# Performance work log

Measured on AMD Instinct MI355X. Metric: run time of the kernel, lower is better.

Reference implementation:

```python
import jax, jax.numpy as jnp
import numpy as np

B, S, H = 4, 2048, 1024
NH, HD = 16, 64
FF = 4096
EPS = 1e-5

def _ln(x, g, b):
    m = jnp.mean(x, axis=-1, keepdims=True)
    v = jnp.var(x, axis=-1, keepdims=True)
    return (x - m) * jax.lax.rsqrt(v + EPS) * g + b

def setup_inputs() -> dict:
    key = jax.random.key(0)
    ks = jax.random.split(key, 12)
    sc = 0.02
    return {
        "hidden_states": jax.random.normal(ks[0], (B, S, H), jnp.float32),
        "Wq": jax.random.normal(ks[1], (H, H), jnp.float32) * sc,
        "bq": jnp.zeros((H,), jnp.float32),
        "Wk": jax.random.normal(ks[2], (H, H), jnp.float32) * sc,
        "bk": jnp.zeros((H,), jnp.float32),
        "Wv": jax.random.normal(ks[3], (H, H), jnp.float32) * sc,
        "bv": jnp.zeros((H,), jnp.float32),
        "Wi": jax.random.normal(ks[4], (H, FF), jnp.float32) * sc,
        "bi": jnp.zeros((FF,), jnp.float32),
        "Wo": jax.random.normal(ks[5], (FF, H), jnp.float32) * sc,
        "bo": jnp.zeros((H,), jnp.float32),
        "g1": jnp.ones((H,), jnp.float32),
        "b1": jnp.zeros((H,), jnp.float32),
        "g2": jnp.ones((H,), jnp.float32),
        "b2": jnp.zeros((H,), jnp.float32),
    }

def reference(hidden_states, Wq, bq, Wk, bk, Wv, bv, Wi, bi, Wo, bo, g1, b1, g2, b2):
    x = hidden_states
    # projections -> [B, NH, S, HD]
    def split(t):
        return t.reshape(B, S, NH, HD).transpose(0, 2, 1, 3)
    q = split(x @ Wq + bq)
    k = split(x @ Wk + bk)
    v = split(x @ Wv + bv)
    scores = jnp.einsum('bhqd,bhkd->bhqk', q, k) / jnp.sqrt(jnp.float32(HD))
    probs = jax.nn.softmax(scores, axis=-1)
    ctx = jnp.einsum('bhqk,bhkd->bhqd', probs, v)
    attn_out = ctx.transpose(0, 2, 1, 3).reshape(B, S, H)
    h = _ln(x + attn_out, g1, b1)
    ffn = jax.nn.gelu(h @ Wi + bi, approximate=False) @ Wo + bo
    return _ln(h + ffn, g2, b2)
```

## Files before the change

kernel.cpp:

```cpp
#include <hip/hip_runtime.h>

#define B_  4
#define S_  2048
#define H_  1024
#define NH_ 16
#define HD_ 64
#define FF_ 4096
#define M_  (B_*S_)

typedef __bf16 bf16x8 __attribute__((ext_vector_type(8)));
typedef float  f32x4  __attribute__((ext_vector_type(4)));
typedef unsigned short ushort8v __attribute__((ext_vector_type(8)));
typedef unsigned short ushort4v __attribute__((ext_vector_type(4)));

typedef __attribute__((address_space(1))) void GVOID;
typedef __attribute__((address_space(3))) void LVOID;

__device__ __forceinline__ void g2l16(const void* g, void* l) {
  __builtin_amdgcn_global_load_lds((GVOID*)g, (LVOID*)l, 16, 0, 0);
}

#define MFMA16(a, b, c) __builtin_amdgcn_mfma_f32_16x16x32_bf16(a, b, c, 0, 0, 0)

#if __has_builtin(__builtin_amdgcn_exp2f)
#define EXP2(x) __builtin_amdgcn_exp2f(x)
#else
#define EXP2(x) exp2f(x)
#endif

__device__ __forceinline__ unsigned short f2bf(float f) {
  unsigned int u = __float_as_uint(f);
  u += 0x7fffu + ((u >> 16) & 1u);
  return (unsigned short)(u >> 16);
}
__device__ __forceinline__ float bf2f(unsigned short h) {
  return __uint_as_float(((unsigned int)h) << 16);
}

__device__ __forceinline__ void xcd_swz(int& bx, int& by) {
  int gx = gridDim.x;
  int flat = by * gx + bx;
  int cpx = (gx * gridDim.y) >> 3;
  int swz = (flat & 7) * cpx + (flat >> 3);
  bx = swz % gx;
  by = swz / gx;
}

__device__ __forceinline__ void xcd_swzT(int& bx, int& by) {
  int gy = gridDim.y;
  int flat = bx * gy + by;
  int cpx = (gridDim.x * gy) >> 3;
  int swz = (flat & 7) * cpx + (flat >> 3);
  by = swz % gy;
  bx = swz / gy;
}

__global__ __launch_bounds__(256) void cast_f32_bf16(const float* __restrict__ in,
                                                     unsigned short* __restrict__ out,
                                                     int n4) {
  int i = blockIdx.x * 256 + threadIdx.x;
  if (i >= n4) return;
  float4 v = reinterpret_cast<const float4*>(in)[i];
  ushort4v o;
  o[0] = f2bf(v.x); o[1] = f2bf(v.y); o[2] = f2bf(v.z); o[3] = f2bf(v.w);
  reinterpret_cast<ushort4v*>(out)[i] = o;
}

__global__ __launch_bounds__(256) void transpose_cast(const float* __restrict__ in,
                                                      unsigned short* __restrict__ out,
                                                      int R, int C) {
  __shared__ float t[32][33];
  const int bx = blockIdx.x * 32;
  const int by = blockIdx.y * 32;
  const int tx = threadIdx.x & 31, ty = threadIdx.x >> 5;
#pragma unroll
  for (int i = 0; i < 32; i += 8)
    t[ty + i][tx] = in[(size_t)(by + ty + i) * C + bx + tx];
  __syncthreads();
#pragma unroll
  for (int i = 0; i < 32; i += 8)
    out[(size_t)(bx + ty + i) * R + by + tx] = f2bf(t[tx][ty + i]);
}

__global__ __launch_bounds__(256) void transpose_cast3(const float* __restrict__ i0,
                                                       const float* __restrict__ i1,
                                                       const float* __restrict__ i2,
                                                       unsigned short* __restrict__ o0,
                                                       unsigned short* __restrict__ o1,
                                                       unsigned short* __restrict__ o2) {
  __shared__ float t[32][33];
  const float* in = (blockIdx.z == 0) ? i0 : (blockIdx.z == 1) ? i1 : i2;
  unsigned short* out = (blockIdx.z == 0) ? o0 : (blockIdx.z == 1) ? o1 : o2;
  const int bx = blockIdx.x * 32;
  const int by = blockIdx.y * 32;
  const int tx = threadIdx.x & 31, ty = threadIdx.x >> 5;
#pragma unroll
  for (int i = 0; i < 32; i += 8)
    t[ty + i][tx] = in[(size_t)(by + ty + i) * H_ + bx + tx];
  __syncthreads();
#pragma unroll
  for (int i = 0; i < 32; i += 8)
    out[(size_t)(bx + ty + i) * H_ + by + tx] = f2bf(t[tx][ty + i]);
}

#define ALOAD(bufv, mf, ks)                                                      \
  *reinterpret_cast<const bf16x8*>((char*)As + (bufv)*32768 + wm*16384 +         \
      ((mf)*16 + lr)*128 + (((((ks)*4 + kg)) ^ (lr & 7)) * 16))
#define BLOAD(bufv, nf, ks)                                                      \
  *reinterpret_cast<const bf16x8*>((char*)Bs + (bufv)*32768 + bh*16384 +         \
      (brow0 + (nf)*16 + lr)*128 + (((((ks)*4 + kg)) ^ (lr & 7)) * 16))

#define PH_MFMA(MF0)                                                             \
  __builtin_amdgcn_s_barrier();                                                  \
  asm volatile("s_waitcnt lgkmcnt(0)" ::: "memory");                             \
  __builtin_amdgcn_s_setprio(1);                                                 \
  _Pragma("unroll")                                                              \
  for (int nf = 0; nf < 4; ++nf) {                                               \
    acc[MF0][nf]     = MFMA16(a_[0][0], bfr[nf][0], acc[MF0][nf]);               \
    acc[MF0][nf]     = MFMA16(a_[0][1], bfr[nf][1], acc[MF0][nf]);               \
    acc[MF0 + 1][nf] = MFMA16(a_[1][0], bfr[nf][0], acc[MF0 + 1][nf]);           \
    acc[MF0 + 1][nf] = MFMA16(a_[1][1], bfr[nf][1], acc[MF0 + 1][nf]);           \
  }                                                                              \
  __builtin_amdgcn_s_setprio(0);

#define GEMM256_CORE(A_, Bt_, LDK_, NKT_, KOFF_)                                 \
  __shared__ unsigned short As[2][2][128 * 64];                                  \
  __shared__ unsigned short Bs[2][2][128 * 64];                                  \
  const int tid  = threadIdx.x;                                                  \
  const int wave = tid >> 6;                                                     \
  const int lane = tid & 63;                                                     \
  const int kg   = lane >> 4;                                                    \
  const int lr   = lane & 15;                                                    \
  const int wm   = wave >> 2;                                                    \
  const int wn   = wave & 3;                                                     \
  const int bh   = wn >> 1;                                                      \
  const int brow0 = (wn & 1) * 64;                                               \
  const int sr = lane >> 3;                                                      \
  const int sc = ((lane & 7) ^ sr) * 8;                                          \
  const unsigned short* sA = &A_[(size_t)(m0 + wave * 8 + sr) * LDK_ + KOFF_ + sc];  \
  const unsigned short* sB = &Bt_[(size_t)(n0 + wave * 8 + sr) * LDK_ + KOFF_ + sc]; \
  char* ldsA = (char*)&As[0][0][0] + wave * 1024;                                \
  char* ldsB = (char*)&Bs[0][0][0] + wave * 1024;                                \
  const size_t rkI = (size_t)64 * LDK_;                                          \
  const size_t rhK = (size_t)128 * LDK_;                                         \
  f32x4 acc[8][4] = {};                                                          \
  const int nkt = (NKT_);                                                        \
  g2l16(sA,             ldsA);                                                   \
  g2l16(sA + rkI,       ldsA + 8192);                                            \
  g2l16(sA + rhK,       ldsA + 16384);                                           \
  g2l16(sA + rhK + rkI, ldsA + 16384 + 8192);                                    \
  g2l16(sB,             ldsB);                                                   \
  g2l16(sB + rkI,       ldsB + 8192);                                            \
  g2l16(sB + rhK,       ldsB + 16384);                                           \
  g2l16(sB + rhK + rkI, ldsB + 16384 + 8192);                                    \
  g2l16(sB + 64,             ldsB + 32768);                                      \
  g2l16(sB + rkI + 64,       ldsB + 32768 + 8192);                               \
  g2l16(sB + rhK + 64,       ldsB + 32768 + 16384);                              \
  g2l16(sB + rhK + rkI + 64, ldsB + 32768 + 16384 + 8192);                       \
  asm volatile("s_waitcnt vmcnt(4)" ::: "memory");                               \
  __builtin_amdgcn_s_barrier();                                                  \
  for (int c = 0; c < nkt; ++c) {                                                \
    const int buf = c & 1;                                                       \
    const bool stgA = (c + 1 < nkt);                                             \
    const bool stgB = (c + 2 < nkt);                                             \
    const size_t kA = (size_t)(c + 1) * 64;                                      \
    const size_t kB = (size_t)(c + 2) * 64;                                      \
    bf16x8 bfr[4][2];                                                            \
    bf16x8 a_[2][2];                                                             \
    _Pragma("unroll")                                                            \
    for (int nf = 0; nf < 4; ++nf) {                                             \
      bfr[nf][0] = BLOAD(buf, nf, 0);                                            \
      bfr[nf][1] = BLOAD(buf, nf, 1);                                            \
    }                                                                            \
    a_[0][0] = ALOAD(buf, 0, 0); a_[0][1] = ALOAD(buf, 0, 1);                    \
    a_[1][0] = ALOAD(buf, 1, 0); a_[1][1] = ALOAD(buf, 1, 1);                    \
    if (stgA) {                                                                  \
      g2l16(sA + kA,       ldsA + (buf ^ 1) * 32768);                            \
      g2l16(sA + rkI + kA, ldsA + (buf ^ 1) * 32768 + 8192);                     \
    }                                                                            \
    PH_MFMA(0)                                                                   \
    __builtin_amdgcn_s_barrier();                                                \
    a_[0][0] = ALOAD(buf, 2, 0); a_[0][1] = ALOAD(buf, 2, 1);                    \
    a_[1][0] = ALOAD(buf, 3, 0); a_[1][1] = ALOAD(buf, 3, 1);                    \
    if (stgA) {                                                                  \
      g2l16(sA + rhK + kA,       ldsA + (buf ^ 1) * 32768 + 16384);              \
      g2l16(sA + rhK + rkI + kA, ldsA + (buf ^ 1) * 32768 + 16384 + 8192);       \
    }                                                                            \
    PH_MFMA(2)                                                                   \
    __builtin_amdgcn_s_barrier();                                                \
    a_[0][0] = ALOAD(buf, 4, 0); a_[0][1] = ALOAD(buf, 4, 1);                    \
    a_[1][0] = ALOAD(buf, 5, 0); a_[1][1] = ALOAD(buf, 5, 1);                    \
    if (stgB) {                                                                  \
      g2l16(sB + kB,       ldsB + buf * 32768);                                  \
      g2l16(sB + rkI + kB, ldsB + buf * 32768 + 8192);                           \
    }                                                                            \
    PH_MFMA(4)                                                                   \
    __builtin_amdgcn_s_barrier();                                                \
    a_[0][0] = ALOAD(buf, 6, 0); a_[0][1] = ALOAD(buf, 6, 1);                    \
    a_[1][0] = ALOAD(buf, 7, 0); a_[1][1] = ALOAD(buf, 7, 1);                    \
    if (stgB) {                                                                  \
      g2l16(sB + rhK + kB,       ldsB + buf * 32768 + 16384);                    \
      g2l16(sB + rhK + rkI + kB, ldsB + buf * 32768 + 16384 + 8192);             \
    }                                                                            \
    PH_MFMA(6)                                                                   \
    if (c < nkt - 2)       asm volatile("s_waitcnt vmcnt(4)" ::: "memory");      \
    else if (c == nkt - 2) asm volatile("s_waitcnt vmcnt(0)" ::: "memory");      \
    __builtin_amdgcn_s_barrier();                                                \
  }

template<int ACT, int OUT_F32>
__global__ __launch_bounds__(512, 1) void gemm256_tn(const unsigned short* __restrict__ A,
                                                     const unsigned short* __restrict__ Bt,
                                                     const float* __restrict__ bias,
                                                     void* __restrict__ C,
                                                     int M, int N, int K) {
  int bx = blockIdx.x, by = blockIdx.y;
  xcd_swzT(bx, by);
  const int z = blockIdx.z;
  const int Klen = K / gridDim.z;
  const int Koff = z * Klen;
  const float* biasEff = (z == 0) ? bias : nullptr;
  const int m0 = bx * 256;
  const int n0 = by * 256;
  GEMM256_CORE(A, Bt, K, Klen >> 6, Koff)

  float* Cf = (float*)C + (size_t)z * M * N;
#pragma unroll
  for (int mf = 0; mf < 8; ++mf) {
#pragma unroll
    for (int nf = 0; nf < 4; ++nf) {
      int col = n0 + wn * 64 + nf * 16 + lr;
      float bc = biasEff ? biasEff[col] : 0.0f;
#pragma unroll
      for (int r = 0; r < 4; ++r) {
        int row = m0 + wm * 128 + mf * 16 + kg * 4 + r;
        float v = acc[mf][nf][r] + bc;
        if (ACT == 1) v = 0.5f * v * (1.0f + erff(v * 0.70710678118f));
        if (OUT_F32) Cf[(size_t)row * N + col] = v;
        else reinterpret_cast<unsigned short*>(C)[(size_t)row * N + col] = f2bf(v);
      }
    }
  }
}

__global__ __launch_bounds__(512, 1) void gemm256_qkv(const unsigned short* __restrict__ A,
                                                      const unsigned short* __restrict__ Bt,
                                                      const float* __restrict__ bq,
                                                      const float* __restrict__ bk,
                                                      const float* __restrict__ bv,
                                                      unsigned short* __restrict__ qb,
                                                      unsigned short* __restrict__ kb,
                                                      unsigned short* __restrict__ vt,
                                                      float qscale) {
  int bx = blockIdx.x, by = blockIdx.y;
  xcd_swzT(bx, by);
  const int m0 = bx * 256;
  const int n0 = by * 256;
  GEMM256_CORE(A, Bt, H_, H_ >> 6, 0)

#pragma unroll
  for (int mf = 0; mf < 8; ++mf) {
#pragma unroll
    for (int nf = 0; nf < 4; ++nf) {
      int colb = n0 + wn * 64 + nf * 16;
      int col  = colb + lr;
      int seg  = colb >> 10;
      int row0 = m0 + wm * 128 + mf * 16 + kg * 4;
      if (seg == 0) {
        float bc = bq[col];
#pragma unroll
        for (int r = 0; r < 4; ++r)
          qb[(size_t)(row0 + r) * H_ + col] = f2bf((acc[mf][nf][r] + bc) * qscale);
      } else if (seg == 1) {
        float bc = bk[col - 1024];
#pragma unroll
        for (int r = 0; r < 4; ++r)
          kb[(size_t)(row0 + r) * H_ + col - 1024] = f2bf(acc[mf][nf][r] + bc);
      } else {
        float bc = bv[col - 2048];
        ushort4v o;
#pragma unroll
        for (int r = 0; r < 4; ++r) o[r] = f2bf(acc[mf][nf][r] + bc);
        *reinterpret_cast<ushort4v*>(&vt[(size_t)(col - 2048) * M_ + row0]) = o;
      }
    }
  }
}

__global__ __launch_bounds__(256) void attn_fwd(const unsigned short* __restrict__ Q,
                                                const unsigned short* __restrict__ Kb,
                                                const unsigned short* __restrict__ VT,
                                                unsigned short* __restrict__ O) {
  __shared__ unsigned short Ks[2][64 * 64];
  __shared__ unsigned short Vs[2][64 * 64];
  __shared__ __bf16 Ps[4][16 * 64];

  const int tid  = threadIdx.x;
  const int wave = tid >> 6;
  const int lane = tid & 63;
  const int kg   = lane >> 4;
  const int lr   = lane & 15;
  int bx = blockIdx.x, by = blockIdx.y;
  xcd_swz(bx, by);
  const int b  = by >> 4;
  const int h  = by & 15;
  const size_t rowbase = (size_t)b * S_;
  const int hcol = h * 64;
  const int bcol0 = b * S_;
  const int q0 = bx * 128 + wave * 32;

  const int rT0 = (wave * 2 + 0) * 8 + (lane >> 3);
  const int rT1 = (wave * 2 + 1) * 8 + (lane >> 3);
  const int ce  = ((lane & 7) * 8) ^ (((lane >> 3) & 7) << 3);
  const int fswz = (lr & 7) << 3;

  bf16x8 qf[2][2];
#pragma unroll
  for (int sub = 0; sub < 2; ++sub)
#pragma unroll
    for (int d = 0; d < 2; ++d)
      qf[sub][d] = *reinterpret_cast<const bf16x8*>(
          &Q[(rowbase + q0 + sub * 16 + lr) * H_ + hcol + d * 32 + kg * 8]);

  bf16x8 ones;
#pragma unroll
  for (int i = 0; i < 8; ++i) ones[i] = (__bf16)1.0f;

  const f32x4 cinit = {-8.0f, -8.0f, -8.0f, -8.0f};

  f32x4 ctx[2][4] = {};
  f32x4 lsum[2] = {};

  auto stage = [&](int kt, int buf) {
    g2l16(&Kb[(rowbase + kt * 64 + rT0) * H_ + hcol + ce], &Ks[buf][(wave * 2 + 0) * 512]);
    g2l16(&Kb[(rowbase + kt * 64 + rT1) * H_ + hcol + ce], &Ks[buf][(wave * 2 + 1) * 512]);
    g2l16(&VT[(size_t)(hcol + rT0) * M_ + bcol0 + kt * 64 + ce], &Vs[buf][(wave * 2 + 0) * 512]);
    g2l16(&VT[(size_t)(hcol + rT1) * M_ + bcol0 + kt * 64 + ce], &Vs[buf][(wave * 2 + 1) * 512]);
  };

  stage(0, 0);
  __syncthreads();

  const int NT = S_ / 64;
  for (int kt = 0; kt < NT; ++kt) {
    const int cur = kt & 1;
    if (kt + 1 < NT) stage(kt + 1, cur ^ 1);

    f32x4 s0[4], s1[4];
    __builtin_amdgcn_s_setprio(1);
#pragma unroll
    for (int nf = 0; nf < 4; ++nf) {
      int row = nf * 16 + lr;
      bf16x8 kf0 = *reinterpret_cast<const bf16x8*>(&Ks[cur][row * 64 + ((kg * 8) ^ fswz)]);
      bf16x8 kf1 = *reinterpret_cast<const bf16x8*>(&Ks[cur][row * 64 + ((32 + kg * 8) ^ fswz)]);
      f32x4 z0 = cinit, z1 = cinit;
      z0 = MFMA16(qf[0][0], kf0, z0);
      z0 = MFMA16(qf[0][1], kf1, z0);
      z1 = MFMA16(qf[1][0], kf0, z1);
      z1 = MFMA16(qf[1][1], kf1, z1);
      s0[nf] = z0;
      s1[nf] = z1;
    }
    __builtin_amdgcn_s_setprio(0);

#pragma unroll
    for (int nf = 0; nf < 4; ++nf)
#pragma unroll
      for (int r = 0; r < 4; ++r) {
        int row = kg * 4 + r;
        Ps[wave][row * 64 + ((nf * 16 + lr) ^ ((row & 7) << 3))] =
            (__bf16)EXP2(s0[nf][r]);
      }
    bf16x8 p00 = *reinterpret_cast<const bf16x8*>(
        &Ps[wave][lr * 64 + ((kg ^ (lr & 7)) << 3)]);
    bf16x8 p01 = *reinterpret_cast<const bf16x8*>(
        &Ps[wave][lr * 64 + (((4 + kg) ^ (lr & 7)) << 3)]);
#pragma unroll
    for (int nf = 0; nf < 4; ++nf)
#pragma unroll
      for (int r = 0; r < 4; ++r) {
        int row = kg * 4 + r;
        Ps[wave][row * 64 + ((nf * 16 + lr) ^ ((row & 7) << 3))] =
            (__bf16)EXP2(s1[nf][r]);
      }
    bf16x8 p10 = *reinterpret_cast<const bf16x8*>(
        &Ps[wave][lr * 64 + ((kg ^ (lr & 7)) << 3)]);
    bf16x8 p11 = *reinterpret_cast<const bf16x8*>(
        &Ps[wave][lr * 64 + (((4 + kg) ^ (lr & 7)) << 3)]);

    __builtin_amdgcn_s_setprio(1);
#pragma unroll
    for (int df = 0; df < 4; ++df) {
      int row = df * 16 + lr;
      bf16x8 vf0 = *reinterpret_cast<const bf16x8*>(&Vs[cur][row * 64 + ((kg * 8) ^ fswz)]);
      bf16x8 vf1 = *reinterpret_cast<const bf16x8*>(&Vs[cur][row * 64 + ((32 + kg * 8) ^ fswz)]);
      ctx[0][df] = MFMA16(p00, vf0, ctx[0][df]);
      ctx[0][df] = MFMA16(p01, vf1, ctx[0][df]);
      ctx[1][df] = MFMA16(p10, vf0, ctx[1][df]);
      ctx[1][df] = MFMA16(p11, vf1, ctx[1][df]);
    }
    lsum[0] = MFMA16(p00, ones, lsum[0]);
    lsum[0] = MFMA16(p01, ones, lsum[0]);
    lsum[1] = MFMA16(p10, ones, lsum[1]);
    lsum[1] = MFMA16(p11, ones, lsum[1]);
    __builtin_amdgcn_s_setprio(0);

    __syncthreads();
  }

#pragma unroll
  for (int sub = 0; sub < 2; ++sub)
#pragma unroll
    for (int r = 0; r < 4; ++r) {
      float rl = 1.0f / lsum[sub][r];
#pragma unroll
      for (int df = 0; df < 4; ++df) {
        float v = ctx[sub][df][r] * rl;
        O[(rowbase + q0 + sub * 16 + kg * 4 + r) * H_ + hcol + df * 16 + lr] = f2bf(v);
      }
    }
}

template<int IN2_BF16, int WRITE_BF16>
__global__ __launch_bounds__(256) void add_ln(const float* __restrict__ X,
                                              const void* __restrict__ Y,
                                              const float* __restrict__ g,
                                              const float* __restrict__ beta,
                                              float* __restrict__ outF,
                                              unsigned short* __restrict__ outB) {
  const int row = blockIdx.x;
  const int tid = threadIdx.x;
  const int wave = tid >> 6, lane = tid & 63;
  __shared__ float red[8];

  float vals[4];
  float s = 0.0f, s2 = 0.0f;
#pragma unroll
  for (int i = 0; i < 4; ++i) {
    int c = i * 256 + tid;
    float v = X[(size_t)row * H_ + c];
    if (IN2_BF16) v += bf2f(reinterpret_cast<const unsigned short*>(Y)[(size_t)row * H_ + c]);
    else          v += reinterpret_cast<const float*>(Y)[(size_t)row * H_ + c];
    vals[i] = v;
    s += v;
    s2 += v * v;
  }
#pragma unroll
  for (int off = 32; off; off >>= 1) { s += __shfl_xor(s, off); s2 += __shfl_xor(s2, off); }
  if (lane == 0) { red[wave * 2] = s; red[wave * 2 + 1] = s2; }
  __syncthreads();
  s  = red[0] + red[2] + red[4] + red[6];
  s2 = red[1] + red[3] + red[5] + red[7];
  float mean = s * (1.0f / H_);
  float var  = s2 * (1.0f / H_) - mean * mean;
  float rstd = rsqrtf(var + 1e-5f);
#pragma unroll
  for (int i = 0; i < 4; ++i) {
    int c = i * 256 + tid;
    float v = (vals[i] - mean) * rstd * g[c] + beta[c];
    if (outF) outF[(size_t)row * H_ + c] = v;
    if (WRITE_BF16) outB[(size_t)row * H_ + c] = f2bf(v);
  }
}

__global__ __launch_bounds__(256) void add_ln3(const float* __restrict__ X,
                                               const float* __restrict__ Y0,
                                               const float* __restrict__ Y1,
                                               const float* __restrict__ g,
                                               const float* __restrict__ beta,
                                               float* __restrict__ outF) {
  const int row = blockIdx.x;
  const int tid = threadIdx.x;
  const int wave = tid >> 6, lane = tid & 63;
  __shared__ float red[8];

  float vals[4];
  float s = 0.0f, s2 = 0.0f;
#pragma unroll
  for (int i = 0; i < 4; ++i) {
    int c = i * 256 + tid;
    size_t idx = (size_t)row * H_ + c;
    float v = X[idx] + Y0[idx] + Y1[idx];
    vals[i] = v;
    s += v;
    s2 += v * v;
  }
#pragma unroll
  for (int off = 32; off; off >>= 1) { s += __shfl_xor(s, off); s2 += __shfl_xor(s2, off); }
  if (lane == 0) { red[wave * 2] = s; red[wave * 2 + 1] = s2; }
  __syncthreads();
  s  = red[0] + red[2] + red[4] + red[6];
  s2 = red[1] + red[3] + red[5] + red[7];
  float mean = s * (1.0f / H_);
  float var  = s2 * (1.0f / H_) - mean * mean;
  float rstd = rsqrtf(var + 1e-5f);
#pragma unroll
  for (int i = 0; i < 4; ++i) {
    int c = i * 256 + tid;
    outF[(size_t)row * H_ + c] = (vals[i] - mean) * rstd * g[c] + beta[c];
  }
}

extern "C" void kernel_launch(void* const* d_in, const int* in_sizes, int n_in,
                              void* d_out, int out_size, void* d_ws, size_t ws_size,
                              hipStream_t stream) {
  const float* x  = (const float*)d_in[0];
  const float* Wq = (const float*)d_in[1];
  const float* bq = (const float*)d_in[2];
  const float* Wk = (const float*)d_in[3];
  const float* bk = (const float*)d_in[4];
  const float* Wv = (const float*)d_in[5];
  const float* bv = (const float*)d_in[6];
  const float* Wi = (const float*)d_in[7];
  const float* bi = (const float*)d_in[8];
  const float* Wo = (const float*)d_in[9];
  const float* bo = (const float*)d_in[10];
  const float* g1 = (const float*)d_in[11];
  const float* b1 = (const float*)d_in[12];
  const float* g2 = (const float*)d_in[13];
  const float* b2 = (const float*)d_in[14];

  unsigned char* ws = (unsigned char*)d_ws;
  size_t off = 0;
  auto alloc = [&](size_t bytes) { size_t o = off; off += (bytes + 255) & ~(size_t)255; return o; };

  unsigned short* WqkvT = (unsigned short*)(ws + alloc((size_t)3 * H_ * H_ * 2));
  unsigned short* WiT   = (unsigned short*)(ws + alloc((size_t)H_ * FF_ * 2));
  unsigned short* WoT   = (unsigned short*)(ws + alloc((size_t)FF_ * H_ * 2));
  float*          hf    = (float*)(ws + alloc((size_t)M_ * H_ * 4));
  unsigned short* hb    = (unsigned short*)(ws + alloc((size_t)M_ * H_ * 2));
  unsigned short* f1    = (unsigned short*)(ws + alloc((size_t)M_ * FF_ * 2));
  unsigned short* xb    = (unsigned short*)(ws + alloc((size_t)M_ * H_ * 2));
  unsigned short* qb    = (unsigned short*)(ws + alloc((size_t)M_ * H_ * 2));
  unsigned short* kb    = (unsigned short*)(ws + alloc((size_t)M_ * H_ * 2));
  unsigned short* vt    = (unsigned short*)(ws + alloc((size_t)M_ * H_ * 2));
  unsigned short* ao    = (unsigned short*)(ws + alloc((size_t)M_ * H_ * 2));
  float*          f2p   = (float*)xb;

  {
    int n4 = (int)((size_t)M_ * H_ / 4);
    cast_f32_bf16<<<(n4 + 255) / 256, 256, 0, stream>>>(x, xb, n4);
  }
  transpose_cast3<<<dim3(H_ / 32, H_ / 32, 3), 256, 0, stream>>>(
      Wq, Wk, Wv, WqkvT, WqkvT + (size_t)H_ * H_, WqkvT + (size_t)2 * H_ * H_);
  transpose_cast<<<dim3(FF_ / 32, H_ / 32), 256, 0, stream>>>(Wi, WiT, H_, FF_);
  transpose_cast<<<dim3(H_ / 32, FF_ / 32), 256, 0, stream>>>(Wo, WoT, FF_, H_);

  const float QSCALE = 0.125f * 1.44269504088896340736f;

  gemm256_qkv<<<dim3(M_ / 256, 3072 / 256), 512, 0, stream>>>(xb, WqkvT, bq, bk, bv,
                                                              qb, kb, vt, QSCALE);

  attn_fwd<<<dim3(S_ / 128, B_ * NH_), 256, 0, stream>>>(qb, kb, vt, ao);

  add_ln<1, 1><<<M_, 256, 0, stream>>>(x, ao, g1, b1, hf, hb);

  gemm256_tn<1, 0><<<dim3(M_ / 256, FF_ / 256), 512, 0, stream>>>(hb, WiT, bi, f1, M_, FF_, H_);
  gemm256_tn<0, 1><<<dim3(M_ / 256, H_ / 256, 2), 512, 0, stream>>>(f1, WoT, bo, f2p, M_, H_, FF_);

  add_ln3<<<M_, 256, 0, stream>>>(hf, f2p, f2p + (size_t)M_ * H_, g2, b2, (float*)d_out);
}
```

Baseline: 457.3 us.

## Use tanh GELU, merge weight transposes, double attention block query rows

Replaces the exact erf GELU in the FFN GEMM epilogue with the tanh approximation built from exp2, which cuts the cost of the epilogue transcendental. Merges the three weight transpose-cast launches into one kernel that decodes its segment from the block id. Doubles the attention block to 512 threads and 256 query rows so each staged K/V tile is shared by eight waves instead of four. The GELU approximation departs from the erf reference and may add numerical error. The larger attention blocks halve the grid size, which could lower occupancy.

```diff
diff --git a/kernel.cpp b/kernel.cpp
--- a/kernel.cpp
+++ b/kernel.cpp
@@ -35,6 +35,13 @@
 }
 __device__ __forceinline__ float bf2f(unsigned short h) {
   return __uint_as_float(((unsigned int)h) << 16);
+}
+
+__device__ __forceinline__ float gelu_fast(float v) {
+  float y = 0.7978845608f * (v + 0.044715f * v * v * v);
+  float e = EXP2(y * 2.8853900818f);
+  float th = 1.0f - 2.0f / (e + 1.0f);
+  return 0.5f * v * (1.0f + th);
 }
 
 __device__ __forceinline__ void xcd_swz(int& bx, int& by) {
@@ -66,12 +73,33 @@
   reinterpret_cast<ushort4v*>(out)[i] = o;
 }
 
-__global__ __launch_bounds__(256) void transpose_cast(const float* __restrict__ in,
-                                                      unsigned short* __restrict__ out,
-                                                      int R, int C) {
+__global__ __launch_bounds__(256) void prep_weights(const float* __restrict__ Wq,
+                                                    const float* __restrict__ Wk,
+                                                    const float* __restrict__ Wv,
+                                                    const float* __restrict__ Wi,
+                                                    const float* __restrict__ Wo,
+                                                    unsigned short* __restrict__ WqkvT,
+                                                    unsigned short* __restrict__ WiT,
+                                                    unsigned short* __restrict__ WoT) {
   __shared__ float t[32][33];
-  const int bx = blockIdx.x * 32;
-  const int by = blockIdx.y * 32;
+  int id = blockIdx.x;
+  const float* in; unsigned short* out; int R, C, bx, by;
+  if (id < 3072) {
+    int seg = id >> 10, rem = id & 1023;
+    in = (seg == 0) ? Wq : (seg == 1) ? Wk : Wv;
+    out = WqkvT + (size_t)seg * H_ * H_;
+    R = H_; C = H_;
+    bx = rem & 31; by = rem >> 5;
+  } else if (id < 3072 + 4096) {
+    int rem = id - 3072;
+    in = Wi; out = WiT; R = H_; C = FF_;
+    bx = rem & 127; by = rem >> 7;
+  } else {
+    int rem = id - 3072 - 4096;
+    in = Wo; out = WoT; R = FF_; C = H_;
+    bx = rem & 31; by = rem >> 5;
+  }
+  bx *= 32; by *= 32;
   const int tx = threadIdx.x & 31, ty = threadIdx.x >> 5;
 #pragma unroll
   for (int i = 0; i < 32; i += 8)
@@ -80,27 +108,6 @@
 #pragma unroll
   for (int i = 0; i < 32; i += 8)
     out[(size_t)(bx + ty + i) * R + by + tx] = f2bf(t[tx][ty + i]);
-}
-
-__global__ __launch_bounds__(256) void transpose_cast3(const float* __restrict__ i0,
-                                                       const float* __restrict__ i1,
-                                                       const float* __restrict__ i2,
-                                                       unsigned short* __restrict__ o0,
-                                                       unsigned short* __restrict__ o1,
-                                                       unsigned short* __restrict__ o2) {
-  __shared__ float t[32][33];
-  const float* in = (blockIdx.z == 0) ? i0 : (blockIdx.z == 1) ? i1 : i2;
-  unsigned short* out = (blockIdx.z == 0) ? o0 : (blockIdx.z == 1) ? o1 : o2;
-  const int bx = blockIdx.x * 32;
-  const int by = blockIdx.y * 32;
-  const int tx = threadIdx.x & 31, ty = threadIdx.x >> 5;
-#pragma unroll
-  for (int i = 0; i < 32; i += 8)
-    t[ty + i][tx] = in[(size_t)(by + ty + i) * H_ + bx + tx];
-  __syncthreads();
-#pragma unroll
-  for (int i = 0; i < 32; i += 8)
-    out[(size_t)(bx + ty + i) * H_ + by + tx] = f2bf(t[tx][ty + i]);
 }
 
 #define ALOAD(bufv, mf, ks)                                                      \
@@ -235,7 +242,7 @@
       for (int r = 0; r < 4; ++r) {
         int row = m0 + wm * 128 + mf * 16 + kg * 4 + r;
         float v = acc[mf][nf][r] + bc;
-        if (ACT == 1) v = 0.5f * v * (1.0f + erff(v * 0.70710678118f));
+        if (ACT == 1) v = gelu_fast(v);
         if (OUT_F32) Cf[(size_t)row * N + col] = v;
         else reinterpret_cast<unsigned short*>(C)[(size_t)row * N + col] = f2bf(v);
       }
@@ -287,13 +294,13 @@
   }
 }
 
-__global__ __launch_bounds__(256) void attn_fwd(const unsigned short* __restrict__ Q,
+__global__ __launch_bounds__(512) void attn_fwd(const unsigned short* __restrict__ Q,
                                                 const unsigned short* __restrict__ Kb,
                                                 const unsigned short* __restrict__ VT,
                                                 unsigned short* __restrict__ O) {
   __shared__ unsigned short Ks[2][64 * 64];
   __shared__ unsigned short Vs[2][64 * 64];
-  __shared__ __bf16 Ps[4][16 * 64];
+  __shared__ __bf16 Ps[8][16 * 64];
 
   const int tid  = threadIdx.x;
   const int wave = tid >> 6;
@@ -307,11 +314,10 @@
   const size_t rowbase = (size_t)b * S_;
   const int hcol = h * 64;
   const int bcol0 = b * S_;
-  const int q0 = bx * 128 + wave * 32;
-
-  const int rT0 = (wave * 2 + 0) * 8 + (lane >> 3);
-  const int rT1 = (wave * 2 + 1) * 8 + (lane >> 3);
-  const int ce  = ((lane & 7) * 8) ^ (((lane >> 3) & 7) << 3);
+  const int q0 = bx * 256 + wave * 32;
+
+  const int rT = wave * 8 + (lane >> 3);
+  const int ce = ((lane & 7) * 8) ^ (((lane >> 3) & 7) << 3);
   const int fswz = (lr & 7) << 3;
 
   bf16x8 qf[2][2];
@@ -332,10 +338,8 @@
   f32x4 lsum[2] = {};
 
   auto stage = [&](int kt, int buf) {
-    g2l16(&Kb[(rowbase + kt * 64 + rT0) * H_ + hcol + ce], &Ks[buf][(wave * 2 + 0) * 512]);
-    g2l16(&Kb[(rowbase + kt * 64 + rT1) * H_ + hcol + ce], &Ks[buf][(wave * 2 + 1) * 512]);
-    g2l16(&VT[(size_t)(hcol + rT0) * M_ + bcol0 + kt * 64 + ce], &Vs[buf][(wave * 2 + 0) * 512]);
-    g2l16(&VT[(size_t)(hcol + rT1) * M_ + bcol0 + kt * 64 + ce], &Vs[buf][(wave * 2 + 1) * 512]);
+    g2l16(&Kb[(rowbase + kt * 64 + rT) * H_ + hcol + ce], &Ks[buf][wave * 512]);
+    g2l16(&VT[(size_t)(hcol + rT) * M_ + bcol0 + kt * 64 + ce], &Vs[buf][wave * 512]);
   };
 
   stage(0, 0);
@@ -541,17 +545,15 @@
     int n4 = (int)((size_t)M_ * H_ / 4);
     cast_f32_bf16<<<(n4 + 255) / 256, 256, 0, stream>>>(x, xb, n4);
   }
-  transpose_cast3<<<dim3(H_ / 32, H_ / 32, 3), 256, 0, stream>>>(
-      Wq, Wk, Wv, WqkvT, WqkvT + (size_t)H_ * H_, WqkvT + (size_t)2 * H_ * H_);
-  transpose_cast<<<dim3(FF_ / 32, H_ / 32), 256, 0, stream>>>(Wi, WiT, H_, FF_);
-  transpose_cast<<<dim3(H_ / 32, FF_ / 32), 256, 0, stream>>>(Wo, WoT, FF_, H_);
+  prep_weights<<<3072 + 4096 + 4096, 256, 0, stream>>>(Wq, Wk, Wv, Wi, Wo,
+                                                       WqkvT, WiT, WoT);
 
   const float QSCALE = 0.125f * 1.44269504088896340736f;
 
   gemm256_qkv<<<dim3(M_ / 256, 3072 / 256), 512, 0, stream>>>(xb, WqkvT, bq, bk, bv,
                                                               qb, kb, vt, QSCALE);
 
-  attn_fwd<<<dim3(S_ / 128, B_ * NH_), 256, 0, stream>>>(qb, kb, vt, ao);
+  attn_fwd<<<dim3(S_ / 256, B_ * NH_), 512, 0, stream>>>(qb, kb, vt, ao);
 
   add_ln<1, 1><<<M_, 256, 0, stream>>>(x, ao, g1, b1, hf, hb);
 
```

Measured after the change: 434.2 us. 1.05x faster.
